# Kernel optimization log

Hardware: AMD Instinct MI355X
Metric: run time of the kernel (lower is better)

The kernel has to match this reference:

```python
import jax, jax.numpy as jnp
import numpy as np

N = 8192
D_IN = 512
D_OUT = 256
K = 16          # k_neighbor
ALPHA = 0.5
BETA = 1.0


def get_M(H, beta, k):
    """Cholesky-whitened kNN Gaussian-kernel graph, symmetrized. H: [N, d]."""
    d = H.shape[1]
    A = beta * jnp.eye(d, dtype=H.dtype) + H.T @ H            # [d, d]
    L = jnp.linalg.cholesky(A)                                # lower, A = L L^T
    # norm_covariance = H @ inv(L).T  ==  (L^{-1} H^T)^T
    Z = jax.scipy.linalg.solve_triangular(L, H.T, lower=True).T  # [N, d]
    sq = jnp.sum(Z * Z, axis=1)
    d2 = sq[:, None] + sq[None, :] - 2.0 * (Z @ Z.T)          # [N, N] squared dists
    neg_d2, idx = jax.lax.top_k(-d2, k)                       # k smallest
    vals = jnp.sqrt(jnp.clip(-neg_d2, 0.0))                   # [N, k]
    sigma = jnp.mean(vals)
    kern = jnp.exp(-(vals * vals) / (2.0 * sigma * sigma))
    n = Z.shape[0]
    rows = jnp.repeat(jnp.arange(n), k)
    M = jnp.zeros((n, n), Z.dtype).at[rows, idx.reshape(-1)].add(kern.reshape(-1))
    return 0.5 * (M + M.T)


def normalize_adj(M):
    deg = jnp.sum(M, axis=1)
    dis = jnp.where(deg > 0, deg ** -0.5, 0.0)
    return dis[:, None] * M * dis[None, :]


def setup_inputs() -> dict:
    key = jax.random.key(0)
    k1, k2, k3, k4 = jax.random.split(key, 4)
    lim1 = float(np.sqrt(6.0 / (D_IN + D_OUT)))
    lim2 = float(np.sqrt(6.0 / (D_OUT + D_OUT)))
    return {
        "x": jax.random.normal(k1, (N, D_IN), dtype=jnp.float32),
        "adj": jax.random.uniform(k2, (N, N), dtype=jnp.float32),
        "weight1": jax.random.uniform(k3, (D_IN, D_OUT), dtype=jnp.float32, minval=-lim1, maxval=lim1),
        "weight2": jax.random.uniform(k4, (D_OUT, D_OUT), dtype=jnp.float32, minval=-lim2, maxval=lim2),
    }


def reference(x, adj, weight1, weight2):
    # stage 1: build whitened kNN graph from detached x
    M1 = get_M(jax.lax.stop_gradient(x), BETA, K)
    new_adj = ALPHA * adj + normalize_adj(M1)
    out = jnp.tanh(new_adj @ (x @ weight1))                   # [N, D_OUT]
    # stage 2: rebuild graph from detached hidden, symmetrize weight2
    M2 = get_M(jax.lax.stop_gradient(out), BETA, K)
    new_adj2 = ALPHA * adj + normalize_adj(M2)
    w2_sym = 0.5 * (weight2 + weight2.T)
    out = jnp.tanh(new_adj2 @ (out @ w2_sym))
    return out
```

## Files before the change

kernel.cpp:

```cpp
#include <hip/hip_runtime.h>
#include <math.h>
#include <float.h>

#define N_TOT 8192
#define KNB 16
#define ALPHA 0.5f
#define PROWS 2048
#define NCH 8

typedef short bf16x8 __attribute__((ext_vector_type(8)));
typedef float f32x4 __attribute__((ext_vector_type(4)));

__device__ inline unsigned short f2bf(float f) {
    unsigned u = __float_as_uint(f);
    u += 0x7fffu + ((u >> 16) & 1u);
    return (unsigned short)(u >> 16);
}
__device__ inline float bf2f(unsigned short h) {
    return __uint_as_float(((unsigned)h) << 16);
}

__global__ __launch_bounds__(256)
void k_ata2(const float* __restrict__ H, double* __restrict__ Apart, int d) {
    __shared__ float Ha[32][33], Hb[32][33];
    int tid = threadIdx.x, tx = tid&15, ty = tid>>4;
    int a0 = blockIdx.y*32, b0 = blockIdx.x*32;
    int n0b = blockIdx.z*(N_TOT/NCH);
    int lrow = tid>>3, lseg = tid&7;
    double acc[2][2];
    acc[0][0]=acc[0][1]=acc[1][0]=acc[1][1]=0.0;
    for (int n0 = n0b; n0 < n0b + N_TOT/NCH; n0 += 32) {
        float4 va = *(const float4*)&H[(long)(n0+lrow)*d + a0 + lseg*4];
        float4 vb = *(const float4*)&H[(long)(n0+lrow)*d + b0 + lseg*4];
        __syncthreads();
        Ha[lrow][lseg*4+0]=va.x; Ha[lrow][lseg*4+1]=va.y;
        Ha[lrow][lseg*4+2]=va.z; Ha[lrow][lseg*4+3]=va.w;
        Hb[lrow][lseg*4+0]=vb.x; Hb[lrow][lseg*4+1]=vb.y;
        Hb[lrow][lseg*4+2]=vb.z; Hb[lrow][lseg*4+3]=vb.w;
        __syncthreads();
        float f00=0.f,f01=0.f,f10=0.f,f11=0.f;
        #pragma unroll
        for (int nn = 0; nn < 32; ++nn) {
            float a0v = Ha[nn][ty*2], a1v = Ha[nn][ty*2+1];
            float b0v = Hb[nn][tx*2], b1v = Hb[nn][tx*2+1];
            f00 = fmaf(a0v,b0v,f00); f01 = fmaf(a0v,b1v,f01);
            f10 = fmaf(a1v,b0v,f10); f11 = fmaf(a1v,b1v,f11);
        }
        acc[0][0]+= (double)f00; acc[0][1]+= (double)f01;
        acc[1][0]+= (double)f10; acc[1][1]+= (double)f11;
    }
    long base = (long)blockIdx.z*d*d;
    #pragma unroll
    for (int i=0;i<2;++i)
        #pragma unroll
        for (int j=0;j<2;++j)
            Apart[base + (long)(a0+ty*2+i)*d + b0+tx*2+j] = acc[i][j];
}

__global__ __launch_bounds__(256)
void k_atared(const double* __restrict__ Apart, double* __restrict__ A,
              int d, double beta) {
    long idx = (long)blockIdx.x*256 + threadIdx.x;
    long dd = (long)d*d;
    double s = 0.0;
    for (int ch = 0; ch < NCH; ++ch) s += Apart[ch*dd + idx];
    int r = (int)(idx / d), c = (int)(idx % d);
    A[idx] = s + ((r==c) ? beta : 0.0);
}

__global__ __launch_bounds__(64)
void k_chol_diag(double* __restrict__ A, int d, int p0) {
    __shared__ double Ad[64][65];
    int r = threadIdx.x;
    for (int idx = r; idx < 64*64; idx += 64)
        Ad[idx>>6][idx&63] = A[(long)(p0+(idx>>6))*d + p0+(idx&63)];
    __syncthreads();
    for (int j = 0; j < 64; ++j) {
        double pj = sqrt(Ad[j][j]);
        double lrj = Ad[r][j] / pj;
        __syncthreads();
        if (r > j) Ad[r][j] = lrj;
        else if (r == j) Ad[j][j] = pj;
        __syncthreads();
        if (r > j)
            for (int k = j+1; k <= r; ++k)
                Ad[r][k] -= lrj * Ad[k][j];
        __syncthreads();
    }
    for (int idx = r; idx < 64*64; idx += 64) {
        int i = idx>>6, c = idx&63;
        A[(long)(p0+i)*d + p0+c] = (c <= i) ? Ad[i][c] : 0.0;
    }
}

__global__ __launch_bounds__(256)
void k_trsm(double* __restrict__ A, int d, int p0) {
    __shared__ double Lp[64][65];
    __shared__ double dg[64];
    int tid = threadIdx.x;
    for (int idx = tid; idx < 64*64; idx += 256) {
        int j = idx>>6, k = idx&63;
        double v = A[(long)(p0+j)*d + p0+k];
        Lp[j][k] = (j > k) ? v : 0.0;
        if (j == k) dg[j] = v;
    }
    __syncthreads();
    int r = p0 + 64 + blockIdx.x*256 + tid;
    if (r >= d) return;
    double* Ar = &A[(long)r*d + p0];
    double v[64];
    #pragma unroll
    for (int j = 0; j < 64; ++j) v[j] = Ar[j];
    #pragma unroll
    for (int k = 0; k < 64; ++k) {
        double lr = v[k] / dg[k];
        Ar[k] = lr;
        #pragma unroll
        for (int j = 0; j < 64; ++j) v[j] -= lr * Lp[j][k];
    }
}

__global__ __launch_bounds__(256)
void k_syrk(double* __restrict__ A, int d, int p0) {
    int t0 = p0 + 64;
    int r0 = t0 + blockIdx.y*64, c0 = t0 + blockIdx.x*64;
    __shared__ double Lr[64][33], Lc[64][33];
    int tid = threadIdx.x, tx = tid&15, ty = tid>>4;
    double acc[16];
    #pragma unroll
    for (int i=0;i<16;++i) acc[i]=0.0;
    for (int kc = 0; kc < 64; kc += 32) {
        for (int idx = tid; idx < 64*32; idx += 256) {
            int i = idx>>5, k = idx&31;
            Lr[i][k] = A[(long)(r0+i)*d + p0+kc+k];
            Lc[i][k] = A[(long)(c0+i)*d + p0+kc+k];
        }
        __syncthreads();
        for (int k = 0; k < 32; ++k) {
            double a[4], b[4];
            #pragma unroll
            for (int i=0;i<4;++i){ a[i]=Lr[ty*4+i][k]; b[i]=Lc[tx*4+i][k]; }
            #pragma unroll
            for (int i=0;i<4;++i)
                #pragma unroll
                for (int j=0;j<4;++j) acc[i*4+j] += a[i]*b[j];
        }
        __syncthreads();
    }
    #pragma unroll
    for (int i=0;i<4;++i)
        #pragma unroll
        for (int j=0;j<4;++j)
            A[(long)(r0+ty*4+i)*d + (c0+tx*4+j)] -= acc[i*4+j];
}

__global__ __launch_bounds__(64)
void k_dinv(const double* __restrict__ A, double* __restrict__ X, int d) {
    __shared__ double Lb[64][65];
    __shared__ double Yb[64][65];
    int b = blockIdx.x, c = threadIdx.x;
    for (int r = 0; r < 64; ++r) Lb[r][c] = A[(long)(b*64+r)*d + b*64+c];
    for (int r = 0; r < 64; ++r) Yb[r][c] = 0.0;
    __syncthreads();
    for (int i = 0; i < 64; ++i) {
        double s = (i==c) ? 1.0 : 0.0;
        for (int k = 0; k < i; ++k) s -= Lb[i][k]*Yb[k][c];
        Yb[i][c] = s / Lb[i][i];
    }
    __syncthreads();
    for (int r = 0; r < 64; ++r) X[(long)(b*64+r)*d + b*64+c] = Yb[r][c];
}

__global__ __launch_bounds__(256)
void k_xoff(const double* __restrict__ A, double* __restrict__ X, int d, int lev) {
    __shared__ double Lb[64][65];
    __shared__ double Xb[64][65];
    __shared__ double Sb[64][65];
    int j = blockIdx.x, i = j + lev;
    int tid = threadIdx.x, tx = tid&15, ty = tid>>4;
    double acc[4][4];
    #pragma unroll
    for (int m=0;m<4;++m)
        #pragma unroll
        for (int n=0;n<4;++n) acc[m][n]=0.0;
    for (int k = j; k < i; ++k) {
        __syncthreads();
        for (int idx = tid; idx < 64*64; idx += 256) {
            int r = idx>>6, cc = idx&63;
            Lb[r][cc] = A[(long)(i*64+r)*d + k*64+cc];
            Xb[r][cc] = X[(long)(k*64+r)*d + j*64+cc];
        }
        __syncthreads();
        for (int kk = 0; kk < 64; ++kk) {
            double a_[4], b_[4];
            #pragma unroll
            for (int m=0;m<4;++m) a_[m] = Lb[ty*4+m][kk];
            #pragma unroll
            for (int n=0;n<4;++n) b_[n] = Xb[kk][tx*4+n];
            #pragma unroll
            for (int m=0;m<4;++m)
                #pragma unroll
                for (int n=0;n<4;++n) acc[m][n] += a_[m]*b_[n];
        }
    }
    __syncthreads();
    #pragma unroll
    for (int m=0;m<4;++m)
        #pragma unroll
        for (int n=0;n<4;++n) Sb[ty*4+m][tx*4+n] = acc[m][n];
    for (int idx = tid; idx < 64*64; idx += 256) {
        int r = idx>>6, cc = idx&63;
        Lb[r][cc] = X[(long)(i*64+r)*d + i*64+cc];
    }
    __syncthreads();
    #pragma unroll
    for (int m=0;m<4;++m)
        #pragma unroll
        for (int n=0;n<4;++n) acc[m][n]=0.0;
    for (int kk = 0; kk < 64; ++kk) {
        double a_[4], b_[4];
        #pragma unroll
        for (int m=0;m<4;++m) a_[m] = Lb[ty*4+m][kk];
        #pragma unroll
        for (int n=0;n<4;++n) b_[n] = Sb[kk][tx*4+n];
        #pragma unroll
        for (int m=0;m<4;++m)
            #pragma unroll
            for (int n=0;n<4;++n) acc[m][n] += a_[m]*b_[n];
    }
    #pragma unroll
    for (int m=0;m<4;++m)
        #pragma unroll
        for (int n=0;n<4;++n)
            X[(long)(i*64+ty*4+m)*d + j*64+tx*4+n] = -acc[m][n];
}

__global__ __launch_bounds__(256)
void k_wtr(const double* __restrict__ X, double* __restrict__ W, int d, int shift) {
    int idx = blockIdx.x*256 + threadIdx.x;
    int k = idx >> shift, c = idx & (d-1);
    W[idx] = (k <= c) ? X[(long)c*d + k] : 0.0;
}

__global__ __launch_bounds__(256)
void k_hw(const float* __restrict__ H, const double* __restrict__ W,
          float* __restrict__ Z, int d) {
    __shared__ __align__(16) float Ht[32][68];
    __shared__ double Wt[32][66];
    int tid = threadIdx.x, tx = tid&15, ty = tid>>4;
    int r0 = blockIdx.y*64, c0 = blockIdx.x*64;
    double acc[4][4];
    #pragma unroll
    for (int i=0;i<4;++i)
        #pragma unroll
        for (int j=0;j<4;++j) acc[i][j]=0.0;
    for (int k0 = 0; k0 < d; k0 += 32) {
        {
            int row = tid>>2, koff = (tid&3)*8;
            const float* src = &H[(long)(r0+row)*d + k0+koff];
            float4 v0 = *(const float4*)src, v1 = *(const float4*)(src+4);
            Ht[koff+0][row]=v0.x; Ht[koff+1][row]=v0.y; Ht[koff+2][row]=v0.z; Ht[koff+3][row]=v0.w;
            Ht[koff+4][row]=v1.x; Ht[koff+5][row]=v1.y; Ht[koff+6][row]=v1.z; Ht[koff+7][row]=v1.w;
        }
        {
            int k = tid>>3, coff = (tid&7)*8;
            const double* src = &W[(long)(k0+k)*d + c0+coff];
            #pragma unroll
            for (int q=0;q<8;++q) Wt[k][coff+q] = src[q];
        }
        __syncthreads();
        #pragma unroll
        for (int k = 0; k < 32; ++k) {
            float4 av = *(const float4*)&Ht[k][ty*4];
            double a0=av.x, a1=av.y, a2=av.z, a3=av.w;
            double b[4];
            #pragma unroll
            for (int j=0;j<4;++j) b[j] = Wt[k][tx*4+j];
            #pragma unroll
            for (int j=0;j<4;++j) {
                acc[0][j] += a0*b[j]; acc[1][j] += a1*b[j];
                acc[2][j] += a2*b[j]; acc[3][j] += a3*b[j];
            }
        }
        __syncthreads();
    }
    #pragma unroll
    for (int i=0;i<4;++i)
        #pragma unroll
        for (int j=0;j<4;++j)
            Z[(long)(r0+ty*4+i)*d + c0+tx*4+j] = (float)acc[i][j];
}

__global__ __launch_bounds__(256)
void k_sq(const float* __restrict__ Z, float* __restrict__ sq, int d) {
    int row = blockIdx.x*4 + (threadIdx.x>>6);
    int lane = threadIdx.x&63;
    const float* z = &Z[(long)row*d];
    double s = 0.0;
    for (int c = lane; c < d; c += 64) { float v = z[c]; s += (double)v*v; }
    #pragma unroll
    for (int off=32; off>0; off>>=1) s += __shfl_down(s, off);
    if (lane==0) sq[row] = (float)s;
}

__global__ __launch_bounds__(256)
void k_bf16(const float* __restrict__ Z, unsigned short* __restrict__ Zh, long n) {
    long i = ((long)blockIdx.x*256 + threadIdx.x)*8;
    if (i >= n) return;
    float4 v0 = *(const float4*)&Z[i], v1 = *(const float4*)&Z[i+4];
    float z[8] = {v0.x,v0.y,v0.z,v0.w,v1.x,v1.y,v1.z,v1.w};
    __align__(16) unsigned short h[8];
    #pragma unroll
    for (int j=0;j<8;++j) h[j] = f2bf(z[j]);
    *(uint4*)&Zh[i] = *(const uint4*)h;
}

__global__ __launch_bounds__(256)
void k_gram(const unsigned short* __restrict__ Zh, const float* __restrict__ sq,
            float* __restrict__ d2, int d, int prow0) {
    __shared__ unsigned short At[128*64], Bt[128*64];
    int tid = threadIdx.x, w = tid>>6, lane = tid&63;
    int lr = lane&15, kg = lane>>4;
    int wr = w>>1, wc = w&1;
    int r0 = prow0 + blockIdx.y*128;
    int c0 = blockIdx.x*128;
    f32x4 acc[4][4];
    #pragma unroll
    for (int m=0;m<4;++m)
        #pragma unroll
        for (int n=0;n<4;++n) acc[m][n] = (f32x4){0.f,0.f,0.f,0.f};

    for (int k0 = 0; k0 < d; k0 += 64) {
        __syncthreads();
        #pragma unroll
        for (int ii=0; ii<4; ++ii) {
            int rbase = w*32 + ii*8;
            int grow = rbase + (lane>>3);
            int gg = (lane&7) ^ (grow&7);
            __builtin_amdgcn_global_load_lds((const void*)&Zh[(long)(r0+grow)*d + k0 + gg*8],
                                             (void*)&At[rbase*64], 16, 0, 0);
            __builtin_amdgcn_global_load_lds((const void*)&Zh[(long)(c0+grow)*d + k0 + gg*8],
                                             (void*)&Bt[rbase*64], 16, 0, 0);
        }
        __syncthreads();
        #pragma unroll
        for (int ks=0; ks<2; ++ks) {
            int gsw = ((ks<<2)|kg) ^ (lr&7);
            bf16x8 a_[4];
            #pragma unroll
            for (int m=0;m<4;++m) a_[m] = *(const bf16x8*)&At[(wr*64+m*16+lr)*64 + gsw*8];
            #pragma unroll
            for (int n=0;n<4;++n) {
                bf16x8 b_ = *(const bf16x8*)&Bt[(wc*64+n*16+lr)*64 + gsw*8];
                #pragma unroll
                for (int m=0;m<4;++m)
                    acc[m][n] = __builtin_amdgcn_mfma_f32_16x16x32_bf16(a_[m], b_, acc[m][n], 0,0,0);
            }
        }
    }
    float sr[4][4];
    #pragma unroll
    for (int m=0;m<4;++m)
        #pragma unroll
        for (int q=0;q<4;++q) sr[m][q] = sq[r0 + wr*64 + m*16 + kg*4 + q];
    #pragma unroll
    for (int n=0;n<4;++n) {
        int col = c0 + wc*64 + n*16 + lr;
        float sc = sq[col];
        #pragma unroll
        for (int m=0;m<4;++m) {
            int rloc = (r0 - prow0) + wr*64 + m*16 + kg*4;
            #pragma unroll
            for (int q=0;q<4;++q)
                d2[(long)(rloc+q)*N_TOT + col] = sr[m][q] + sc - 2.f*acc[m][n][q];
        }
    }
}

__global__ __launch_bounds__(256)
void k_sel(const float* __restrict__ d2, int* __restrict__ tI32, int prow0) {
    __shared__ float cbv[320];
    __shared__ int   cbi[320];
    __shared__ int   red[4];
    __shared__ int   cnt_s;
    __shared__ float fD[32];
    __shared__ int   fI[32];
    int tid = threadIdx.x, w = tid>>6, lane = tid&63;
    int row = blockIdx.x;
    const float* rp = &d2[(long)row*N_TOT];
    float v[32];
    #pragma unroll
    for (int j=0;j<8;++j) {
        float4 q = *(const float4*)&rp[j*1024 + tid*4];
        v[j*4+0]=q.x; v[j*4+1]=q.y; v[j*4+2]=q.z; v[j*4+3]=q.w;
    }
    unsigned u[32];
    #pragma unroll
    for (int i=0;i<32;++i) {
        unsigned b = __float_as_uint(v[i]);
        u[i] = (b & 0x80000000u) ? ~b : (b | 0x80000000u);
    }
    unsigned p = 0;
    for (int b = 31; b >= 0; --b) {
        unsigned t = p | (1u<<b);
        int c = 0;
        #pragma unroll
        for (int i=0;i<32;++i) c += (u[i] < t) ? 1 : 0;
        #pragma unroll
        for (int off=1; off<64; off<<=1) c += __shfl_xor(c, off);
        if (lane == 0) red[w] = c;
        __syncthreads();
        c = red[0]+red[1]+red[2]+red[3];
        if (c < 32) p = t;
        __syncthreads();
    }
    if (tid == 0) cnt_s = 0;
    __syncthreads();
    #pragma unroll
    for (int i=0;i<32;++i) {
        if (u[i] <= p) {
            int pos = atomicAdd(&cnt_s, 1);
            if (pos < 320) { cbv[pos] = v[i]; cbi[pos] = (i>>2)*1024 + tid*4 + (i&3); }
        }
    }
    __syncthreads();
    if (tid == 0) {
        int m = cnt_s; if (m > 320) m = 320;
        #pragma unroll
        for (int k=0;k<32;++k){ fD[k]=FLT_MAX; fI[k]=k; }
        for (int t = 0; t < m; ++t) {
            float dv = cbv[t]; int ci = cbi[t];
            float wd = fD[31]; int wi = fI[31];
            if (dv < wd || (dv == wd && ci < wi)) {
                int pos = 31;
                while (pos > 0) {
                    float pd_=fD[pos-1]; int pi_=fI[pos-1];
                    if (dv < pd_ || (dv == pd_ && ci < pi_)) { fD[pos]=pd_; fI[pos]=pi_; --pos; }
                    else break;
                }
                fD[pos]=dv; fI[pos]=ci;
            }
        }
        long rg = (long)(prow0 + row);
        #pragma unroll
        for (int k=0;k<32;++k) tI32[rg*32 + k] = fI[k];
    }
}

template<int D>
__global__ __launch_bounds__(256)
void k_refine(const float* __restrict__ Z, const float* __restrict__ sq,
              const int* __restrict__ tI32,
              float* __restrict__ tD, int* __restrict__ tI, double* sig_accum) {
    __shared__ float rD[4][32];
    __shared__ int   rI[4][32];
    __shared__ float bD[4][17];
    __shared__ int   bI[4][17];
    int wv = threadIdx.x>>6, lane = threadIdx.x&63;
    long row = (long)blockIdx.x*4 + wv;
    float zi[D/64];
    #pragma unroll
    for (int t=0;t<D/64;++t) zi[t] = Z[row*D + t*64 + lane];
    float sqi = sq[row];
    for (int c = 0; c < 32; ++c) {
        int j = tI32[row*32 + c];
        float dot = 0.f;
        #pragma unroll
        for (int t=0;t<D/64;++t) dot = fmaf(zi[t], Z[(long)j*D + t*64 + lane], dot);
        #pragma unroll
        for (int off=32; off>0; off>>=1) dot += __shfl_xor(dot, off);
        if (lane == 0) { rD[wv][c] = sqi + sq[j] - 2.f*dot; rI[wv][c] = j; }
    }
    if (lane == 0) {
        #pragma unroll
        for (int k=0;k<16;++k){ bD[wv][k]=FLT_MAX; bI[wv][k]=0x7fffffff; }
        for (int c = 0; c < 32; ++c) {
            float dv = rD[wv][c]; int ci = rI[wv][c];
            float wd = bD[wv][15]; int wi = bI[wv][15];
            if (dv < wd || (dv == wd && ci < wi)) {
                int pos = 15;
                while (pos > 0) {
                    float pd_ = bD[wv][pos-1]; int pi_ = bI[wv][pos-1];
                    if (dv < pd_ || (dv == pd_ && ci < pi_)) {
                        bD[wv][pos]=pd_; bI[wv][pos]=pi_; --pos;
                    } else break;
                }
                bD[wv][pos]=dv; bI[wv][pos]=ci;
            }
        }
        double ps = 0.0;
        #pragma unroll
        for (int k=0;k<16;++k) {
            float dv = bD[wv][k];
            tD[row*16+k] = dv; tI[row*16+k] = bI[wv][k];
            ps += sqrt((double)fmaxf(dv, 0.f));
        }
        atomicAdd(sig_accum, ps);
    }
}

__global__ void k_sigfin(const double* __restrict__ sig_accum, float* __restrict__ inv2s2) {
    double s = sig_accum[0] / (double)(N_TOT*KNB);
    inv2s2[0] = (float)(1.0/(2.0*s*s));
}

__global__ __launch_bounds__(256)
void k_kern(const float* __restrict__ tD, const int* __restrict__ tI,
            const float* __restrict__ inv2s2,
            float* __restrict__ kern, float* __restrict__ deg) {
    int e = blockIdx.x*256 + threadIdx.x;
    int i = e>>4;
    float d2 = fmaxf(tD[e], 0.f);
    float kv = expf(-d2 * inv2s2[0]);
    kern[e] = kv;
    atomicAdd(&deg[i], 0.5f*kv);
    atomicAdd(&deg[tI[e]], 0.5f*kv);
}

__global__ __launch_bounds__(256)
void k_dis(const float* __restrict__ deg, float* __restrict__ dis) {
    int i = blockIdx.x*256 + threadIdx.x;
    float v = deg[i];
    dis[i] = (v > 0.f) ? (1.0f/sqrtf(v)) : 0.f;
}

__global__ __launch_bounds__(256)
void k_count(const int* __restrict__ tI, int* __restrict__ cnt) {
    int e = blockIdx.x*256 + threadIdx.x;
    atomicAdd(&cnt[tI[e]], 1);
}

__global__ __launch_bounds__(1024)
void k_scan(const int* __restrict__ cnt, int* __restrict__ rowstart) {
    __shared__ int buf[1024];
    __shared__ int carry;
    int tid = threadIdx.x;
    if (tid==0) carry = 0;
    __syncthreads();
    for (int base = 0; base < N_TOT; base += 1024) {
        int v = cnt[base+tid];
        buf[tid]=v; __syncthreads();
        for (int off=1; off<1024; off<<=1) {
            int t = (tid>=off)? buf[tid-off] : 0; __syncthreads();
            buf[tid]+=t; __syncthreads();
        }
        rowstart[base+tid] = carry + buf[tid] - v;
        __syncthreads();
        if (tid==1023) carry += buf[1023];
        __syncthreads();
    }
    if (tid==0) rowstart[N_TOT] = carry;
}

__global__ __launch_bounds__(256)
void k_fill(const int* __restrict__ tI, const float* __restrict__ kern,
            const int* __restrict__ rowstart, int* __restrict__ c2,
            int* __restrict__ in_src, float* __restrict__ in_w) {
    int e = blockIdx.x*256 + threadIdx.x;
    int i = e>>4;
    int j = tI[e];
    int pos = atomicAdd(&c2[j], 1);
    int dst = rowstart[j] + pos;
    in_src[dst] = i; in_w[dst] = kern[e];
}

__global__ __launch_bounds__(256)
void k_gemm(const float* __restrict__ A, const float* __restrict__ B,
            float* __restrict__ C, int M, int N, int Kd, float scale) {
    __shared__ __align__(16) float At[16][68];
    __shared__ __align__(16) float Bt[16][68];
    int tid = threadIdx.x, tx = tid&15, ty = tid>>4;
    int r0 = blockIdx.y*64, c0 = blockIdx.x*64;
    float acc[4][4];
    #pragma unroll
    for (int i=0;i<4;++i)
        #pragma unroll
        for (int j=0;j<4;++j) acc[i][j]=0.f;
    for (int k0 = 0; k0 < Kd; k0 += 16) {
        {
            int row = tid>>2, koff = (tid&3)*4;
            float4 v = *(const float4*)&A[(long)(r0+row)*Kd + k0+koff];
            At[koff+0][row]=v.x; At[koff+1][row]=v.y; At[koff+2][row]=v.z; At[koff+3][row]=v.w;
        }
        {
            int k = tid>>4, coff = (tid&15)*4;
            float4 v = *(const float4*)&B[(long)(k0+k)*N + c0+coff];
            *(float4*)&Bt[k][coff] = v;
        }
        __syncthreads();
        #pragma unroll
        for (int k=0;k<16;++k) {
            float4 a = *(const float4*)&At[k][ty*4];
            float4 b = *(const float4*)&Bt[k][tx*4];
            float ar[4] = {a.x,a.y,a.z,a.w};
            float br[4] = {b.x,b.y,b.z,b.w};
            #pragma unroll
            for (int i=0;i<4;++i)
                #pragma unroll
                for (int j=0;j<4;++j) acc[i][j] = fmaf(ar[i], br[j], acc[i][j]);
        }
        __syncthreads();
    }
    #pragma unroll
    for (int i=0;i<4;++i)
        #pragma unroll
        for (int j=0;j<4;++j)
            C[(long)(r0+ty*4+i)*N + c0+tx*4+j] = scale*acc[i][j];
}

__global__ __launch_bounds__(256)
void k_prepPT(const float* __restrict__ P, unsigned short* __restrict__ PTsh,
              unsigned short* __restrict__ PTsl) {
    __shared__ float tile[64][65];
    int r0 = blockIdx.y*64;
    int c0 = blockIdx.x*64;
    int t = threadIdx.x;
    {
        int row = t>>2, cseg = t&3;
        #pragma unroll
        for (int i=0;i<4;++i) {
            float4 v = *(const float4*)&P[(long)(r0+row)*256 + c0 + cseg*16 + i*4];
            tile[row][cseg*16+i*4+0]=v.x; tile[row][cseg*16+i*4+1]=v.y;
            tile[row][cseg*16+i*4+2]=v.z; tile[row][cseg*16+i*4+3]=v.w;
        }
    }
    __syncthreads();
    {
        int col = t>>2, rseg = t&3;
        int c = c0 + col;
        __align__(16) unsigned short hs[16], ls[16];
        #pragma unroll
        for (int i=0;i<16;++i) {
            float z = tile[rseg*16+i][col];
            hs[i] = f2bf(z);
            ls[i] = f2bf(z - bf2f(hs[i]));
        }
        #pragma unroll
        for (int half=0; half<2; ++half) {
            int gl = rseg*2 + half;
            int gs = gl ^ (c&7);
            long dst = (long)c*N_TOT + r0 + gs*8;
            *(uint4*)&PTsh[dst] = *(const uint4*)&hs[half*8];
            *(uint4*)&PTsl[dst] = *(const uint4*)&ls[half*8];
        }
    }
}

__global__ __launch_bounds__(256)
void k_adjP2(const float* __restrict__ adj, const unsigned short* __restrict__ PTsh,
             const unsigned short* __restrict__ PTsl, float* __restrict__ C, float scale) {
    __shared__ unsigned short Ah[64*64], Al[64*64];
    __shared__ unsigned short Bh[128*64], Bl[128*64];
    int tid = threadIdx.x, w = tid>>6, lane = tid&63;
    int lr = lane&15, kg = lane>>4;
    int r0 = blockIdx.y*64;
    int c0 = blockIdx.x*128;
    f32x4 acc[8];
    #pragma unroll
    for (int fc=0; fc<8; ++fc) acc[fc] = (f32x4){0.f,0.f,0.f,0.f};

    int arow = tid>>2, aseg = tid&3;
    for (int k0 = 0; k0 < N_TOT; k0 += 64) {
        __syncthreads();
        {
            const float* asrc = &adj[(long)(r0+arow)*N_TOT + k0 + aseg*16];
            #pragma unroll
            for (int i=0;i<4;++i) {
                float4 v = *(const float4*)&asrc[i*4];
                float z[4] = {v.x,v.y,v.z,v.w};
                __align__(8) unsigned short h[4], l[4];
                #pragma unroll
                for (int j=0;j<4;++j) {
                    h[j] = f2bf(z[j]);
                    l[j] = f2bf(z[j] - bf2f(h[j]));
                }
                int col = aseg*16 + i*4;
                int g = col>>3, sub = col&7;
                int off = arow*128 + ((g ^ (arow&7))*16) + sub*2;
                *(ushort4*)((char*)Ah + off) = *(const ushort4*)h;
                *(ushort4*)((char*)Al + off) = *(const ushort4*)l;
            }
        }
        #pragma unroll
        for (int ii=0; ii<4; ++ii) {
            int rbase = w*32 + ii*8;
            int grow = rbase + (lane>>3);
            long src = (long)(c0+grow)*N_TOT + k0 + (lane&7)*8;
            __builtin_amdgcn_global_load_lds((const void*)&PTsh[src], (void*)&Bh[rbase*64], 16, 0, 0);
            __builtin_amdgcn_global_load_lds((const void*)&PTsl[src], (void*)&Bl[rbase*64], 16, 0, 0);
        }
        __syncthreads();
        #pragma unroll
        for (int ks=0; ks<2; ++ks) {
            int gsw = ((ks<<2)|kg) ^ (lr&7);
            bf16x8 ah = *(const bf16x8*)&Ah[(w*16+lr)*64 + gsw*8];
            bf16x8 al = *(const bf16x8*)&Al[(w*16+lr)*64 + gsw*8];
            #pragma unroll
            for (int fc=0; fc<8; ++fc) {
                bf16x8 bh = *(const bf16x8*)&Bh[(fc*16+lr)*64 + gsw*8];
                bf16x8 bl = *(const bf16x8*)&Bl[(fc*16+lr)*64 + gsw*8];
                acc[fc] = __builtin_amdgcn_mfma_f32_16x16x32_bf16(ah, bh, acc[fc], 0,0,0);
                acc[fc] = __builtin_amdgcn_mfma_f32_16x16x32_bf16(ah, bl, acc[fc], 0,0,0);
                acc[fc] = __builtin_amdgcn_mfma_f32_16x16x32_bf16(al, bh, acc[fc], 0,0,0);
            }
        }
    }
    #pragma unroll
    for (int fc=0; fc<8; ++fc)
        #pragma unroll
        for (int q=0; q<4; ++q) {
            int rg = r0 + w*16 + kg*4 + q;
            int cg = c0 + fc*16 + lr;
            C[(long)rg*256 + cg] = scale*acc[fc][q];
        }
}

__global__ __launch_bounds__(256)
void k_wsym(const float* __restrict__ w2, float* __restrict__ w2s) {
    int i = blockIdx.x, j = threadIdx.x;
    w2s[i*256+j] = 0.5f*(w2[i*256+j] + w2[j*256+i]);
}

__global__ __launch_bounds__(256)
void k_spmm_tanh(const float* __restrict__ P, const float* __restrict__ preS,
                 const float* __restrict__ kern, const int* __restrict__ tI,
                 const float* __restrict__ dis, const int* __restrict__ rowstart,
                 const int* __restrict__ in_src, const float* __restrict__ in_w,
                 float* __restrict__ out) {
    int i = blockIdx.x, c = threadIdx.x;
    float acc = 0.f;
    float di = dis[i];
    #pragma unroll 1
    for (int k = 0; k < 16; ++k) {
        int e = i*16+k;
        int j = tI[e];
        float w = 0.5f*kern[e]*dis[j];
        acc = fmaf(w, P[(long)j*256 + c], acc);
    }
    int s0 = rowstart[i], s1 = rowstart[i+1];
    for (int t = s0; t < s1; ++t) {
        int j = in_src[t];
        float w = 0.5f*in_w[t]*dis[j];
        acc = fmaf(w, P[(long)j*256 + c], acc);
    }
    float pre = preS[(long)i*256+c] + di*acc;
    out[(long)i*256+c] = tanhf(pre);
}

extern "C" void kernel_launch(void* const* d_in, const int* in_sizes, int n_in,
                              void* d_out, int out_size, void* d_ws, size_t ws_size,
                              hipStream_t stream) {
    const float* x   = (const float*)d_in[0];
    const float* adj = (const float*)d_in[1];
    const float* w1  = (const float*)d_in[2];
    const float* w2  = (const float*)d_in[3];

    char* ws = (char*)d_ws;
    size_t off = 0;
    auto alloc = [&](size_t bytes){ size_t o = off; off += (bytes+255)&~(size_t)255; return o; };
    double* A      = (double*)(ws + alloc((size_t)512*512*8));
    double* W      = (double*)(ws + alloc((size_t)512*512*8));
    double* Xb     = (double*)(ws + alloc((size_t)512*512*8));
    double* Apart  = (double*)(ws + alloc((size_t)NCH*512*512*8));
    double* sigacc = (double*)(ws + alloc(256));
    float*  inv2s2 = (float*)(ws + alloc(256));
    float*  bigZ   = (float*)(ws + alloc((size_t)N_TOT*512*4));
    unsigned short* Zh   = (unsigned short*)(ws + alloc((size_t)N_TOT*512*2));
    unsigned short* PTsh = (unsigned short*)(ws + alloc((size_t)256*N_TOT*2));
    unsigned short* PTsl = (unsigned short*)(ws + alloc((size_t)256*N_TOT*2));
    float*  d2buf  = (float*)(ws + alloc((size_t)PROWS*N_TOT*4));
    float*  sq     = (float*)(ws + alloc((size_t)N_TOT*4));
    int*    tI32   = (int*)  (ws + alloc((size_t)N_TOT*32*4));
    float*  tD     = (float*)(ws + alloc((size_t)N_TOT*16*4));
    int*    tI     = (int*)  (ws + alloc((size_t)N_TOT*16*4));
    float*  kern   = (float*)(ws + alloc((size_t)N_TOT*16*4));
    float*  deg    = (float*)(ws + alloc((size_t)N_TOT*4));
    float*  dis    = (float*)(ws + alloc((size_t)N_TOT*4));
    int*    cnt    = (int*)  (ws + alloc((size_t)N_TOT*4));
    int*    rowstart=(int*)  (ws + alloc((size_t)(N_TOT+1)*4));
    int*    c2     = (int*)  (ws + alloc((size_t)N_TOT*4));
    int*    in_src = (int*)  (ws + alloc((size_t)N_TOT*16*4));
    float*  in_w   = (float*)(ws + alloc((size_t)N_TOT*16*4));
    float*  out1   = (float*)(ws + alloc((size_t)N_TOT*256*4));
    float*  w2s    = (float*)(ws + alloc((size_t)256*256*4));
    float*  P      = bigZ;
    float*  preS   = bigZ + (size_t)N_TOT*256;

    auto run_stage = [&](const float* H, int d, const float* Bmat, float* outBuf) {
        int nb = d/64;
        int shift = (d == 512) ? 9 : 8;
        k_ata2<<<dim3(d/32, d/32, NCH), 256, 0, stream>>>(H, Apart, d);
        k_atared<<<d*d/256, 256, 0, stream>>>(Apart, A, d, 1.0);
        for (int p0 = 0; p0 < d; p0 += 64) {
            k_chol_diag<<<1, 64, 0, stream>>>(A, d, p0);
            int rem = d - p0 - 64;
            if (rem > 0) {
                k_trsm<<<(rem+255)/256, 256, 0, stream>>>(A, d, p0);
                k_syrk<<<dim3(rem/64, rem/64), 256, 0, stream>>>(A, d, p0);
            }
        }
        k_dinv<<<nb, 64, 0, stream>>>(A, Xb, d);
        for (int lev = 1; lev < nb; ++lev)
            k_xoff<<<nb - lev, 256, 0, stream>>>(A, Xb, d, lev);
        k_wtr<<<d*d/256, 256, 0, stream>>>(Xb, W, d, shift);
        k_hw<<<dim3(d/64, N_TOT/64), 256, 0, stream>>>(H, W, bigZ, d);
        k_sq<<<N_TOT/4, 256, 0, stream>>>(bigZ, sq, d);
        k_bf16<<<(int)(((long)N_TOT*d)/(256*8)), 256, 0, stream>>>(bigZ, Zh, (long)N_TOT*d);
        for (int pr = 0; pr < N_TOT; pr += PROWS) {
            k_gram<<<dim3(N_TOT/128, PROWS/128), 256, 0, stream>>>(Zh, sq, d2buf, d, pr);
            k_sel<<<PROWS, 256, 0, stream>>>(d2buf, tI32, pr);
        }
        hipMemsetAsync(sigacc, 0, 8, stream);
        if (d == 512)
            k_refine<512><<<N_TOT/4, 256, 0, stream>>>(bigZ, sq, tI32, tD, tI, sigacc);
        else
            k_refine<256><<<N_TOT/4, 256, 0, stream>>>(bigZ, sq, tI32, tD, tI, sigacc);
        k_sigfin<<<1, 1, 0, stream>>>(sigacc, inv2s2);
        hipMemsetAsync(deg, 0, N_TOT*4, stream);
        k_kern<<<N_TOT*16/256, 256, 0, stream>>>(tD, tI, inv2s2, kern, deg);
        k_dis<<<N_TOT/256, 256, 0, stream>>>(deg, dis);
        hipMemsetAsync(cnt, 0, N_TOT*4, stream);
        k_count<<<N_TOT*16/256, 256, 0, stream>>>(tI, cnt);
        k_scan<<<1, 1024, 0, stream>>>(cnt, rowstart);
        hipMemsetAsync(c2, 0, N_TOT*4, stream);
        k_fill<<<N_TOT*16/256, 256, 0, stream>>>(tI, kern, rowstart, c2, in_src, in_w);
        k_gemm<<<dim3(256/64, N_TOT/64), 256, 0, stream>>>(H, Bmat, P, N_TOT, 256, d, 1.0f);
        k_prepPT<<<dim3(4, N_TOT/64), 256, 0, stream>>>(P, PTsh, PTsl);
        k_adjP2<<<dim3(2, N_TOT/64), 256, 0, stream>>>(adj, PTsh, PTsl, preS, ALPHA);
        k_spmm_tanh<<<N_TOT, 256, 0, stream>>>(P, preS, kern, tI, dis, rowstart,
                                               in_src, in_w, outBuf);
    };

    run_stage(x, 512, w1, out1);
    k_wsym<<<256, 256, 0, stream>>>(w2, w2s);
    run_stage(out1, 256, w2s, (float*)d_out);
}
```

Measured before the change: 5.845 ms.

## Split adj@P GEMM along K with partial buffers and register prefetch of adj

The dense adj@P kernel now splits the 8192-long reduction into four slices via a z grid dimension, which raises the block count from 256 to 1024 so all CUs on the device are used. Each slice writes a partial result, and a new reduction kernel sums the four partials and applies the alpha scale. The kernel also prefetches the next adj tile into registers while the current tile's MFMAs run. In exchange it adds 32 MB of partial-buffer traffic, one extra launch, and a change in float summation order.

```diff
diff --git a/kernel.cpp b/kernel.cpp
--- a/kernel.cpp
+++ b/kernel.cpp
@@ -7,6 +7,7 @@
 #define ALPHA 0.5f
 #define PROWS 2048
 #define NCH 8
+#define KS 4
 
 typedef short bf16x8 __attribute__((ext_vector_type(8)));
 typedef float f32x4 __attribute__((ext_vector_type(4)));
@@ -647,39 +648,42 @@
 }
 
 __global__ __launch_bounds__(256)
-void k_adjP2(const float* __restrict__ adj, const unsigned short* __restrict__ PTsh,
-             const unsigned short* __restrict__ PTsl, float* __restrict__ C, float scale) {
+void k_adjP3(const float* __restrict__ adj, const unsigned short* __restrict__ PTsh,
+             const unsigned short* __restrict__ PTsl, float* __restrict__ part) {
     __shared__ unsigned short Ah[64*64], Al[64*64];
     __shared__ unsigned short Bh[128*64], Bl[128*64];
     int tid = threadIdx.x, w = tid>>6, lane = tid&63;
     int lr = lane&15, kg = lane>>4;
     int r0 = blockIdx.y*64;
     int c0 = blockIdx.x*128;
+    int kbeg = blockIdx.z*(N_TOT/KS), kend = kbeg + N_TOT/KS;
     f32x4 acc[8];
     #pragma unroll
     for (int fc=0; fc<8; ++fc) acc[fc] = (f32x4){0.f,0.f,0.f,0.f};
 
     int arow = tid>>2, aseg = tid&3;
-    for (int k0 = 0; k0 < N_TOT; k0 += 64) {
-        __syncthreads();
-        {
-            const float* asrc = &adj[(long)(r0+arow)*N_TOT + k0 + aseg*16];
-            #pragma unroll
-            for (int i=0;i<4;++i) {
-                float4 v = *(const float4*)&asrc[i*4];
-                float z[4] = {v.x,v.y,v.z,v.w};
-                __align__(8) unsigned short h[4], l[4];
-                #pragma unroll
-                for (int j=0;j<4;++j) {
-                    h[j] = f2bf(z[j]);
-                    l[j] = f2bf(z[j] - bf2f(h[j]));
-                }
-                int col = aseg*16 + i*4;
-                int g = col>>3, sub = col&7;
-                int off = arow*128 + ((g ^ (arow&7))*16) + sub*2;
-                *(ushort4*)((char*)Ah + off) = *(const ushort4*)h;
-                *(ushort4*)((char*)Al + off) = *(const ushort4*)l;
+    float4 va[4];
+    {
+        const float* asrc = &adj[(long)(r0+arow)*N_TOT + kbeg + aseg*16];
+        #pragma unroll
+        for (int i=0;i<4;++i) va[i] = *(const float4*)&asrc[i*4];
+    }
+    for (int k0 = kbeg; k0 < kend; k0 += 64) {
+        __syncthreads();
+        #pragma unroll
+        for (int i=0;i<4;++i) {
+            float z[4] = {va[i].x, va[i].y, va[i].z, va[i].w};
+            __align__(8) unsigned short h[4], l[4];
+            #pragma unroll
+            for (int j=0;j<4;++j) {
+                h[j] = f2bf(z[j]);
+                l[j] = f2bf(z[j] - bf2f(h[j]));
             }
+            int col = aseg*16 + i*4;
+            int g = col>>3, sub = col&7;
+            int off = arow*128 + ((g ^ (arow&7))*16) + sub*2;
+            *(ushort4*)((char*)Ah + off) = *(const ushort4*)h;
+            *(ushort4*)((char*)Al + off) = *(const ushort4*)l;
         }
         #pragma unroll
         for (int ii=0; ii<4; ++ii) {
@@ -690,6 +694,11 @@
             __builtin_amdgcn_global_load_lds((const void*)&PTsl[src], (void*)&Bl[rbase*64], 16, 0, 0);
         }
         __syncthreads();
+        if (k0 + 64 < kend) {
+            const float* asrc = &adj[(long)(r0+arow)*N_TOT + k0 + 64 + aseg*16];
+            #pragma unroll
+            for (int i=0;i<4;++i) va[i] = *(const float4*)&asrc[i*4];
+        }
         #pragma unroll
         for (int ks=0; ks<2; ++ks) {
             int gsw = ((ks<<2)|kg) ^ (lr&7);
@@ -705,14 +714,31 @@
             }
         }
     }
+    long base = (long)blockIdx.z*N_TOT*256;
     #pragma unroll
     for (int fc=0; fc<8; ++fc)
         #pragma unroll
         for (int q=0; q<4; ++q) {
             int rg = r0 + w*16 + kg*4 + q;
             int cg = c0 + fc*16 + lr;
-            C[(long)rg*256 + cg] = scale*acc[fc][q];
-        }
+            part[base + (long)rg*256 + cg] = acc[fc][q];
+        }
+}
+
+__global__ __launch_bounds__(256)
+void k_adjred(const float* __restrict__ part, float* __restrict__ preS, float scale) {
+    long i4 = ((long)blockIdx.x*256 + threadIdx.x)*4;
+    long n = (long)N_TOT*256;
+    float4 a = *(const float4*)&part[i4];
+    float4 b = *(const float4*)&part[n + i4];
+    float4 c = *(const float4*)&part[2*n + i4];
+    float4 d = *(const float4*)&part[3*n + i4];
+    float4 o;
+    o.x = scale*(((a.x + b.x) + c.x) + d.x);
+    o.y = scale*(((a.y + b.y) + c.y) + d.y);
+    o.z = scale*(((a.z + b.z) + c.z) + d.z);
+    o.w = scale*(((a.w + b.w) + c.w) + d.w);
+    *(float4*)&preS[i4] = o;
 }
 
 __global__ __launch_bounds__(256)
@@ -769,6 +795,7 @@
     unsigned short* PTsh = (unsigned short*)(ws + alloc((size_t)256*N_TOT*2));
     unsigned short* PTsl = (unsigned short*)(ws + alloc((size_t)256*N_TOT*2));
     float*  d2buf  = (float*)(ws + alloc((size_t)PROWS*N_TOT*4));
+    float*  part   = (float*)(ws + alloc((size_t)KS*N_TOT*256*4));
     float*  sq     = (float*)(ws + alloc((size_t)N_TOT*4));
     int*    tI32   = (int*)  (ws + alloc((size_t)N_TOT*32*4));
     float*  tD     = (float*)(ws + alloc((size_t)N_TOT*16*4));
@@ -826,7 +853,8 @@
         k_fill<<<N_TOT*16/256, 256, 0, stream>>>(tI, kern, rowstart, c2, in_src, in_w);
         k_gemm<<<dim3(256/64, N_TOT/64), 256, 0, stream>>>(H, Bmat, P, N_TOT, 256, d, 1.0f);
         k_prepPT<<<dim3(4, N_TOT/64), 256, 0, stream>>>(P, PTsh, PTsl);
-        k_adjP2<<<dim3(2, N_TOT/64), 256, 0, stream>>>(adj, PTsh, PTsl, preS, ALPHA);
+        k_adjP3<<<dim3(2, N_TOT/64, KS), 256, 0, stream>>>(adj, PTsh, PTsl, part);
+        k_adjred<<<(N_TOT*256)/(256*4), 256, 0, stream>>>(part, preS, ALPHA);
         k_spmm_tanh<<<N_TOT, 256, 0, stream>>>(P, preS, kern, tI, dis, rowstart,
                                                in_src, in_w, outBuf);
     };
```

Measured after the change: 5.677 ms. 2.9% less time.
